# Kernel optimization log

Hardware: AMD Instinct MI355X
Metric: run time of the kernel (lower is better)

Reference implementation:

```python
import jax, jax.numpy as jnp
import numpy as np

PAD = 10000.0  # sentinel value marking invalid fg points


def setup_inputs() -> dict:
    key = jax.random.key(0)
    k1, k2, k3 = jax.random.split(key, 3)
    B, N, M, D = 8, 4096, 4096, 3
    fg = jax.random.normal(k1, (B, N, D), dtype=jnp.float32)
    prj = jax.random.normal(k2, (B, M, D), dtype=jnp.float32)
    # per-sample valid lengths in [1, N]; pad the tail rows with the sentinel
    x_lengths = jax.random.randint(k3, (B,), 1, N + 1)
    row_idx = jnp.arange(N)[None, :]              # [1, N]
    pad_mask = row_idx >= x_lengths[:, None]      # [B, N] True where padded
    fg = jnp.where(pad_mask[:, :, None], PAD, fg)
    return {"fg_points": fg, "prj_points": prj, "x_lengths": x_lengths}


def _chamfer(fg, prj):
    # fg: [B, N, 3] (padded with PAD rows), prj: [B, M, 3]
    valid = jnp.all(fg != PAD, axis=-1)  # [B, N]
    # squared pairwise distances via ||a||^2 + ||b||^2 - 2 a.b  -> [B, N, M]
    d2 = (jnp.sum(fg * fg, axis=-1)[:, :, None]
          + jnp.sum(prj * prj, axis=-1)[:, None, :]
          - 2.0 * jnp.einsum('bnd,bmd->bnm', fg, prj))
    d2 = jnp.maximum(d2, 0.0)
    n_valid = jnp.sum(valid, axis=1).astype(jnp.float32)  # [B]
    # x -> y: min over prj for each valid fg point, mean over valid points
    cham_x = jnp.sum(jnp.where(valid, jnp.min(d2, axis=2), 0.0), axis=1) / n_valid
    # y -> x: min over valid fg points for each prj point, mean over prj
    BIG = jnp.float32(1e30)
    cham_y = jnp.mean(jnp.min(jnp.where(valid[:, :, None], d2, BIG), axis=1), axis=1)
    # pytorch3d chamfer_distance (default reductions) = cham_x + cham_y per sample
    return jnp.mean(cham_x + cham_y)


def reference(fg_points, prj_points, x_lengths):
    fg = fg_points.astype(jnp.float32)
    prj = prj_points.astype(jnp.float32)
    _ = x_lengths.astype(jnp.int64)  # cast, unused (matches original)
    return _chamfer(fg, prj)
```

## Files before the change

kernel.cpp:

```cpp
#include <hip/hip_runtime.h>

#define TPB 64
#define PPT 8
#define WAVE_OWN (TPB * PPT)
#define CHUNK 128


__global__ __launch_bounds__(TPB, 4) void cham_dist_kernel(
    const float* __restrict__ fg, const float* __restrict__ prj,
    const int* __restrict__ lengths,
    unsigned int* __restrict__ rowmin, unsigned int* __restrict__ colmin,
    int B, int N, int M,
    int tilesX, int chunksX, int tilesY, int chunksY)
{
    const int blocksX = B * tilesX * chunksX;
    int idx = blockIdx.x;
    const int side = (idx >= blocksX) ? 1 : 0;
    if (side) idx -= blocksX;
    const int tilesPer  = side ? tilesY  : tilesX;
    const int chunksPer = side ? chunksY : chunksX;
    const int b     = idx / (tilesPer * chunksPer);
    const int rem   = idx % (tilesPer * chunksPer);
    const int tile  = rem / chunksPer;
    const int chunk = rem % chunksPer;

    const float* own     = side ? prj : fg;
    const float* other   = side ? fg  : prj;
    unsigned int* outArr = side ? colmin : rowmin;
    const int ownCount   = side ? M : N;
    const int otherCount = side ? N : M;
    const int L          = lengths[b];

    const int wbase = tile * WAVE_OWN;
    if (wbase >= ownCount) return;
    if (side == 0 && wbase >= L) return;

    const int start = chunk * CHUNK;
    int cnt = min(CHUNK, otherCount - start);
    if (side == 1) {
        if (start >= L) return;
        cnt = min(cnt, L - start);
    }

    const int lane = threadIdx.x;

    __shared__ float4 tilebuf[CHUNK];
    for (int t = lane; t < cnt; t += TPB) {
        const float* q = other + ((size_t)b * otherCount + start + t) * 3;
        float bx = q[0], by = q[1], bz = q[2];
        tilebuf[t] = make_float4(bx, by, bz, bx * bx + by * by + bz * bz);
    }

    const int lim = side ? ownCount : min(ownCount, L);
    float m2x[PPT], m2y[PPT], m2z[PPT], aa[PPT], mn[PPT];
    #pragma unroll
    for (int p = 0; p < PPT; ++p) {
        int i  = wbase + p * 64 + lane;
        int li = min(i, ownCount - 1);
        const float* a = own + ((size_t)b * ownCount + li) * 3;
        float ax = a[0], ay = a[1], az = a[2];
        m2x[p] = -2.f * ax; m2y[p] = -2.f * ay; m2z[p] = -2.f * az;
        aa[p]  = ax * ax + ay * ay + az * az;
        mn[p]  = __int_as_float(0x7F800000);
    }
    __syncthreads();

    int j = 0;
    for (; j + 3 < cnt; j += 4) {
        float4 q0 = tilebuf[j];
        float4 q1 = tilebuf[j + 1];
        float4 q2 = tilebuf[j + 2];
        float4 q3 = tilebuf[j + 3];
        #pragma unroll
        for (int p = 0; p < PPT; ++p) {
            float t0 = fmaf(m2x[p], q0.x, q0.w);
            t0 = fmaf(m2y[p], q0.y, t0);
            t0 = fmaf(m2z[p], q0.z, t0);
            float t1 = fmaf(m2x[p], q1.x, q1.w);
            t1 = fmaf(m2y[p], q1.y, t1);
            t1 = fmaf(m2z[p], q1.z, t1);
            mn[p] = fminf(fminf(t0, t1), mn[p]);
            float t2 = fmaf(m2x[p], q2.x, q2.w);
            t2 = fmaf(m2y[p], q2.y, t2);
            t2 = fmaf(m2z[p], q2.z, t2);
            float t3 = fmaf(m2x[p], q3.x, q3.w);
            t3 = fmaf(m2y[p], q3.y, t3);
            t3 = fmaf(m2z[p], q3.z, t3);
            mn[p] = fminf(fminf(t2, t3), mn[p]);
        }
    }
    for (; j < cnt; ++j) {
        float4 q0 = tilebuf[j];
        #pragma unroll
        for (int p = 0; p < PPT; ++p) {
            float t0 = fmaf(m2x[p], q0.x, q0.w);
            t0 = fmaf(m2y[p], q0.y, t0);
            t0 = fmaf(m2z[p], q0.z, t0);
            mn[p] = fminf(mn[p], t0);
        }
    }

    #pragma unroll
    for (int p = 0; p < PPT; ++p) {
        int i = wbase + p * 64 + lane;
        if (i < lim) {
            float v = fmaxf(mn[p] + aa[p], 0.f);
            atomicMin(&outArr[(size_t)b * ownCount + i], __float_as_uint(v));
        }
    }
}

#define RSUB 8
#define RTPB 256
__global__ __launch_bounds__(RTPB) void cham_reduce_kernel(
    const unsigned int* __restrict__ rowmin, const unsigned int* __restrict__ colmin,
    const int* __restrict__ lengths, float* __restrict__ out, int B, int N, int M)
{
    __shared__ float wavesum[RTPB / 64];
    const int b    = blockIdx.x / RSUB;
    const int sub  = blockIdx.x % RSUB;
    const int tid  = threadIdx.x;
    const int lane = tid & 63;
    const int wave = tid >> 6;
    const int t      = sub * RTPB + tid;
    const int STRIDE = RSUB * RTPB;

    const int L = lengths[b];
    float sx = 0.f, sy = 0.f;
    for (int n = t; n < L; n += STRIDE) sx += __uint_as_float(rowmin[(size_t)b * N + n]);
    for (int m = t; m < M; m += STRIDE) sy += __uint_as_float(colmin[(size_t)b * M + m]);
    float v = sx / (float)L + sy / (float)M;
    #pragma unroll
    for (int off = 32; off > 0; off >>= 1) v += __shfl_down(v, off, 64);
    if (lane == 0) wavesum[wave] = v;
    __syncthreads();
    if (tid == 0) {
        float tsum = 0.f;
        #pragma unroll
        for (int w = 0; w < RTPB / 64; ++w) tsum += wavesum[w];
        atomicAdd(out, tsum / (float)B);
    }
}

extern "C" void kernel_launch(void* const* d_in, const int* in_sizes, int n_in,
                              void* d_out, int out_size, void* d_ws, size_t ws_size,
                              hipStream_t stream) {
    const float* fg      = (const float*)d_in[0];
    const float* prj     = (const float*)d_in[1];
    const int*   lengths = (const int*)d_in[2];
    float*       out     = (float*)d_out;

    const int B = in_sizes[2];
    const int N = in_sizes[0] / (3 * B);
    const int M = in_sizes[1] / (3 * B);

    unsigned int* rowmin = (unsigned int*)d_ws;
    unsigned int* colmin = rowmin + (size_t)B * N;

    const int tilesX  = (N + WAVE_OWN - 1) / WAVE_OWN;
    const int chunksX = (M + CHUNK - 1) / CHUNK;
    const int tilesY  = (M + WAVE_OWN - 1) / WAVE_OWN;
    const int chunksY = (N + CHUNK - 1) / CHUNK;
    const int totalBlocks = B * (tilesX * chunksX + tilesY * chunksY);
    cham_dist_kernel<<<totalBlocks, TPB, 0, stream>>>(
        fg, prj, lengths, rowmin, colmin, B, N, M, tilesX, chunksX, tilesY, chunksY);

    cham_reduce_kernel<<<B * RSUB, RTPB, 0, stream>>>(rowmin, colmin, lengths, out, B, N, M);
}
```

Measured before the change: 78.13 us.

## Replace atomicMin with per-chunk partial slots reduced in the second kernel

```diff
diff --git a/kernel.cpp b/kernel.cpp
--- a/kernel.cpp
+++ b/kernel.cpp
@@ -9,7 +9,7 @@
 __global__ __launch_bounds__(TPB, 4) void cham_dist_kernel(
     const float* __restrict__ fg, const float* __restrict__ prj,
     const int* __restrict__ lengths,
-    unsigned int* __restrict__ rowmin, unsigned int* __restrict__ colmin,
+    unsigned int* __restrict__ rowslots, unsigned int* __restrict__ colslots,
     int B, int N, int M,
     int tilesX, int chunksX, int tilesY, int chunksY)
 {
@@ -26,7 +26,7 @@
 
     const float* own     = side ? prj : fg;
     const float* other   = side ? fg  : prj;
-    unsigned int* outArr = side ? colmin : rowmin;
+    unsigned int* slots  = side ? colslots : rowslots;
     const int ownCount   = side ? M : N;
     const int otherCount = side ? N : M;
     const int L          = lengths[b];
@@ -100,12 +100,13 @@
         }
     }
 
+    const size_t sbase = ((size_t)b * chunksPer + chunk) * (size_t)ownCount;
     #pragma unroll
     for (int p = 0; p < PPT; ++p) {
         int i = wbase + p * 64 + lane;
         if (i < lim) {
             float v = fmaxf(mn[p] + aa[p], 0.f);
-            atomicMin(&outArr[(size_t)b * ownCount + i], __float_as_uint(v));
+            slots[sbase + i] = __float_as_uint(v);
         }
     }
 }
@@ -113,8 +114,9 @@
 #define RSUB 8
 #define RTPB 256
 __global__ __launch_bounds__(RTPB) void cham_reduce_kernel(
-    const unsigned int* __restrict__ rowmin, const unsigned int* __restrict__ colmin,
-    const int* __restrict__ lengths, float* __restrict__ out, int B, int N, int M)
+    const unsigned int* __restrict__ rowslots, const unsigned int* __restrict__ colslots,
+    const int* __restrict__ lengths, float* __restrict__ out,
+    int B, int N, int M, int chunksX, int chunksY)
 {
     __shared__ float wavesum[RTPB / 64];
     const int b    = blockIdx.x / RSUB;
@@ -127,8 +129,24 @@
 
     const int L = lengths[b];
     float sx = 0.f, sy = 0.f;
-    for (int n = t; n < L; n += STRIDE) sx += __uint_as_float(rowmin[(size_t)b * N + n]);
-    for (int m = t; m < M; m += STRIDE) sy += __uint_as_float(colmin[(size_t)b * M + m]);
+    {
+        const unsigned int* base = rowslots + (size_t)b * chunksX * N;
+        for (int n = t; n < L; n += STRIDE) {
+            unsigned int u = base[n];
+            for (int c = 1; c < chunksX; ++c)
+                u = min(u, base[(size_t)c * N + n]);
+            sx += __uint_as_float(u);
+        }
+    }
+    {
+        const unsigned int* base = colslots + (size_t)b * chunksY * M;
+        for (int m = t; m < M; m += STRIDE) {
+            unsigned int u = base[m];
+            for (int c = 1; c < chunksY; ++c)
+                u = min(u, base[(size_t)c * M + m]);
+            sy += __uint_as_float(u);
+        }
+    }
     float v = sx / (float)L + sy / (float)M;
     #pragma unroll
     for (int off = 32; off > 0; off >>= 1) v += __shfl_down(v, off, 64);
@@ -154,16 +172,18 @@
     const int N = in_sizes[0] / (3 * B);
     const int M = in_sizes[1] / (3 * B);
 
-    unsigned int* rowmin = (unsigned int*)d_ws;
-    unsigned int* colmin = rowmin + (size_t)B * N;
-
     const int tilesX  = (N + WAVE_OWN - 1) / WAVE_OWN;
     const int chunksX = (M + CHUNK - 1) / CHUNK;
     const int tilesY  = (M + WAVE_OWN - 1) / WAVE_OWN;
     const int chunksY = (N + CHUNK - 1) / CHUNK;
+
+    unsigned int* rowslots = (unsigned int*)d_ws;
+    unsigned int* colslots = rowslots + (size_t)B * chunksX * N;
+
     const int totalBlocks = B * (tilesX * chunksX + tilesY * chunksY);
     cham_dist_kernel<<<totalBlocks, TPB, 0, stream>>>(
-        fg, prj, lengths, rowmin, colmin, B, N, M, tilesX, chunksX, tilesY, chunksY);
+        fg, prj, lengths, rowslots, colslots, B, N, M, tilesX, chunksX, tilesY, chunksY);
 
-    cham_reduce_kernel<<<B * RSUB, RTPB, 0, stream>>>(rowmin, colmin, lengths, out, B, N, M);
+    cham_reduce_kernel<<<B * RSUB, RTPB, 0, stream>>>(
+        rowslots, colslots, lengths, out, B, N, M, chunksX, chunksY);
 }
```

Measured after the change: 111.7 us. 1.43x slower.
